# Kernel tuning notes

Hardware: AMD Instinct MI355X
Metric: run time of the kernel (lower is better)

The kernel has to match this reference:

```python
import jax, jax.numpy as jnp
import numpy as np

EMB_DIM = 768
N_WIRES = 10  # (768 - 1).bit_length()
DIM = 2 ** N_WIRES  # 1024
BATCH = 32
SENT_LEN = 128


def _cz_ring_sign(n):
    # Diagonal of (ring of adjacent CZ gates) @ CZ(0, n-1): -1 where an odd
    # number of the qubit pairs (k,k+1) for k<n-1 plus (0,n-1) are both |1>.
    idx = np.arange(2 ** n)
    bits = (idx[:, None] >> (n - 1 - np.arange(n))) & 1  # wire 0 = MSB (kron order)
    par = bits[:, 0] * bits[:, n - 1]
    for k in range(n - 1):
        par = par + bits[:, k] * bits[:, k + 1]
    return jnp.asarray(np.where(par % 2 == 1, -1.0, 1.0).astype(np.complex64))


_CZ_SIGN = _cz_ring_sign(N_WIRES)


def _apply_wire_gates(state, gates):
    # state: (batch, 2**n) complex64; gates: (n, 2, 2) complex64.
    # Contract each 2x2 gate onto its wire instead of building the 2^n x 2^n kron.
    n = gates.shape[0]
    b = state.shape[0]
    v = state.reshape((b,) + (2,) * n)
    for k in range(n):
        v = jnp.moveaxis(v, 1 + k, -1)
        v = v @ gates[k].T  # new_i = sum_j G[i, j] * old_j
        v = jnp.moveaxis(v, -1, 1 + k)
    return v.reshape(b, -1)


def _circuit(s, theta_x, theta_y):
    # [RXLayer, RYLayer, CZRing] repeated 3 times with SHARED parameters
    # (ModuleList([a,b,c]*3) reuses the same module instances).
    cx, sx = jnp.cos(theta_x), jnp.sin(theta_x)
    gx = jnp.stack([jnp.stack([cx, -1j * sx], -1),
                    jnp.stack([-1j * sx, cx], -1)], -2).astype(jnp.complex64)  # (n,2,2)
    cy, sy = jnp.cos(theta_y), jnp.sin(theta_y)
    gy = jnp.stack([jnp.stack([cy, -sy], -1),
                    jnp.stack([sy, cy], -1)], -2).astype(jnp.complex64)  # (n,2,2)
    for _ in range(3):
        s = _apply_wire_gates(s, gx)
        s = _apply_wire_gates(s, gy)
        s = s * _CZ_SIGN  # CZ ring + distant CZ(0, n-1) is diagonal
    return s


def setup_inputs() -> dict:
    key = jax.random.key(0)
    k1, k2, k3 = jax.random.split(key, 3)
    return {
        "x": jax.random.normal(k1, (BATCH, SENT_LEN, EMB_DIM), dtype=jnp.float32),
        "theta_x": jax.random.uniform(k2, (N_WIRES,), dtype=jnp.float32),
        "theta_y": jax.random.uniform(k3, (N_WIRES,), dtype=jnp.float32),
    }


def reference(x, theta_x, theta_y):
    xc = x.astype(jnp.complex64)
    pad = DIM - EMB_DIM
    s = jnp.pad(jnp.mean(xc, axis=1), ((0, 0), (0, pad)))  # (b, 2^n)
    ham = jnp.einsum('bsi,bsj->bij', xc, xc) / xc.shape[1]  # no conj, as in torch
    ham = jnp.pad(ham, ((0, 0), (0, pad), (0, pad)))  # (b, 2^n, 2^n)
    e = _circuit(s, theta_x, theta_y)  # (b, 2^n) complex
    scores = jnp.real(jnp.einsum('bi,bij,bj->b', e, ham, jnp.conj(e)))
    scores = jnp.clip(scores, 0.0, 1.0)
    return scores, e
```

## Files before the change

### kernel.cpp

```cpp
#include <hip/hip_runtime.h>

#define BATCH 32
#define SLEN  128
#define EMB   768
#define DIM   1024
#define NW    10

__global__ void __launch_bounds__(1024) fused_kernel(
        const float* __restrict__ x, const float* __restrict__ tx,
        const float* __restrict__ ty, float* __restrict__ out, int interleaved) {
    __shared__ float re[DIM], im[DIM];
    __shared__ float cx[NW], sx[NW], cy[NW], sy[NW];
    __shared__ float part[16];
    int b = blockIdx.x, t = threadIdx.x;

    if (t < NW) {
        float a = tx[t]; cx[t] = cosf(a); sx[t] = sinf(a);
        float c = ty[t]; cy[t] = cosf(c); sy[t] = sinf(c);
    }

    if (t < EMB) {
        const float* xp = x + (size_t)b * SLEN * EMB + t;
        float s0 = 0.f, s1 = 0.f, s2 = 0.f, s3 = 0.f;
        #pragma unroll 8
        for (int s = 0; s < SLEN; s += 4) {
            s0 += xp[(size_t)(s + 0) * EMB];
            s1 += xp[(size_t)(s + 1) * EMB];
            s2 += xp[(size_t)(s + 2) * EMB];
            s3 += xp[(size_t)(s + 3) * EMB];
        }
        re[t] = (s0 + s1 + s2 + s3) * (1.0f / SLEN);
    } else {
        re[t] = 0.f;
    }
    im[t] = 0.f;
    __syncthreads();

    for (int rep = 0; rep < 3; ++rep) {
        for (int k = 0; k < NW; ++k) {
            if (t < 512) {
                int p = 9 - k;
                int i0 = ((t >> p) << (p + 1)) | (t & ((1 << p) - 1));
                int i1 = i0 | (1 << p);
                float c = cx[k], s = sx[k];
                float r0 = re[i0], m0 = im[i0], r1 = re[i1], m1 = im[i1];
                re[i0] = c * r0 + s * m1;  im[i0] = c * m0 - s * r1;
                re[i1] = c * r1 + s * m0;  im[i1] = c * m1 - s * r0;
            }
            __syncthreads();
        }
        for (int k = 0; k < NW; ++k) {
            if (t < 512) {
                int p = 9 - k;
                int i0 = ((t >> p) << (p + 1)) | (t & ((1 << p) - 1));
                int i1 = i0 | (1 << p);
                float c = cy[k], s = sy[k];
                float r0 = re[i0], m0 = im[i0], r1 = re[i1], m1 = im[i1];
                re[i0] = c * r0 - s * r1;  im[i0] = c * m0 - s * m1;
                re[i1] = s * r0 + c * r1;  im[i1] = s * m0 + c * m1;
            }
            __syncthreads();
        }
        {
            int par = __popc((t & (t >> 1)) & 0x1FF) + ((t & (t >> 9)) & 1);
            if (par & 1) { re[t] = -re[t]; im[t] = -im[t]; }
        }
        __syncthreads();
    }

    float* e_out = out + BATCH;
    if (interleaved) {
        ((float2*)e_out)[b * DIM + t] = make_float2(re[t], im[t]);
    } else {
        e_out[b * DIM + t] = re[t];
    }

    int w = t >> 6, l = t & 63;
    float local = 0.f;
    for (int si = 0; si < 8; ++si) {
        int s = w * 8 + si;
        const float* xr = x + ((size_t)b * SLEN + s) * EMB;
        float du = 0.f, dv = 0.f;
        #pragma unroll
        for (int j = 0; j < 12; ++j) {
            float xv = xr[l + 64 * j];
            du += xv * re[l + 64 * j];
            dv += xv * im[l + 64 * j];
        }
        #pragma unroll
        for (int off = 32; off; off >>= 1) {
            du += __shfl_down(du, off, 64);
            dv += __shfl_down(dv, off, 64);
        }
        if (l == 0) local += du * du + dv * dv;
    }
    if (l == 0) part[w] = local;
    __syncthreads();
    if (t == 0) {
        float a = 0.f;
        #pragma unroll
        for (int i = 0; i < 16; ++i) a += part[i];
        out[b] = fminf(fmaxf(a * (1.0f / SLEN), 0.f), 1.f);
    }
}

extern "C" void kernel_launch(void* const* d_in, const int* in_sizes, int n_in,
                              void* d_out, int out_size, void* d_ws, size_t ws_size,
                              hipStream_t stream) {
    const float* x  = (const float*)d_in[0];
    const float* tx = (const float*)d_in[1];
    const float* ty = (const float*)d_in[2];
    float* out = (float*)d_out;

    int e_elems = out_size - BATCH;
    int interleaved = (e_elems >= BATCH * DIM * 2) ? 1 : 0;

    fused_kernel<<<BATCH, 1024, 0, stream>>>(x, tx, ty, out, interleaved);
}
```

Before: 87.14 us.

## Keep quantum state in registers and apply gates via wavefront shuffles with transposes

Each thread now holds one complex amplitude in registers. Gates on the five low-order qubits are applied with cross-lane shuffles, and the high-order qubits are handled by transposing the state through padded (skewed) shared memory. This replaces about 60 block-wide barriers per block with a few transpose barriers and halves idle threads. The final score loop also caches the state in registers instead of rereading shared memory. The cost is more complex index logic and relying on the wave64 shuffle width covering 32-lane groups.

Result: faster. 83.45 us (-4.2%).

```diff
diff --git a/kernel.cpp b/kernel.cpp
--- a/kernel.cpp
+++ b/kernel.cpp
@@ -6,19 +6,22 @@
 #define DIM   1024
 #define NW    10
 
+__device__ __forceinline__ int skew(int i) { return i + (i >> 5); }
+
 __global__ void __launch_bounds__(1024) fused_kernel(
         const float* __restrict__ x, const float* __restrict__ tx,
         const float* __restrict__ ty, float* __restrict__ out, int interleaved) {
-    __shared__ float re[DIM], im[DIM];
-    __shared__ float cx[NW], sx[NW], cy[NW], sy[NW];
+    __shared__ float2 st[DIM + DIM / 32];
+    __shared__ float cxs[NW], sxs[NW], cys[NW], sys[NW];
     __shared__ float part[16];
     int b = blockIdx.x, t = threadIdx.x;
 
     if (t < NW) {
-        float a = tx[t]; cx[t] = cosf(a); sx[t] = sinf(a);
-        float c = ty[t]; cy[t] = cosf(c); sy[t] = sinf(c);
+        float a = tx[t]; cxs[t] = cosf(a); sxs[t] = sinf(a);
+        float c = ty[t]; cys[t] = cosf(c); sys[t] = sinf(c);
     }
 
+    float r = 0.f, m = 0.f;
     if (t < EMB) {
         const float* xp = x + (size_t)b * SLEN * EMB + t;
         float s0 = 0.f, s1 = 0.f, s2 = 0.f, s3 = 0.f;
@@ -29,53 +32,77 @@
             s2 += xp[(size_t)(s + 2) * EMB];
             s3 += xp[(size_t)(s + 3) * EMB];
         }
-        re[t] = (s0 + s1 + s2 + s3) * (1.0f / SLEN);
-    } else {
-        re[t] = 0.f;
+        r = (s0 + s1 + s2 + s3) * (1.0f / SLEN);
     }
-    im[t] = 0.f;
     __syncthreads();
 
+    int tt = ((t & 31) << 5) | (t >> 5);
+
     for (int rep = 0; rep < 3; ++rep) {
-        for (int k = 0; k < NW; ++k) {
-            if (t < 512) {
-                int p = 9 - k;
-                int i0 = ((t >> p) << (p + 1)) | (t & ((1 << p) - 1));
-                int i1 = i0 | (1 << p);
-                float c = cx[k], s = sx[k];
-                float r0 = re[i0], m0 = im[i0], r1 = re[i1], m1 = im[i1];
-                re[i0] = c * r0 + s * m1;  im[i0] = c * m0 - s * r1;
-                re[i1] = c * r1 + s * m0;  im[i1] = c * m1 - s * r0;
-            }
-            __syncthreads();
+        #pragma unroll
+        for (int p = 0; p < 5; ++p) {
+            float c = cxs[9 - p], s = sxs[9 - p];
+            float pr = __shfl_xor(r, 1 << p, 64);
+            float pm = __shfl_xor(m, 1 << p, 64);
+            float nr = c * r + s * pm, nm = c * m - s * pr;
+            r = nr; m = nm;
         }
-        for (int k = 0; k < NW; ++k) {
-            if (t < 512) {
-                int p = 9 - k;
-                int i0 = ((t >> p) << (p + 1)) | (t & ((1 << p) - 1));
-                int i1 = i0 | (1 << p);
-                float c = cy[k], s = sy[k];
-                float r0 = re[i0], m0 = im[i0], r1 = re[i1], m1 = im[i1];
-                re[i0] = c * r0 - s * r1;  im[i0] = c * m0 - s * m1;
-                re[i1] = s * r0 + c * r1;  im[i1] = s * m0 + c * m1;
-            }
-            __syncthreads();
+        st[skew(t)] = make_float2(r, m);
+        __syncthreads();
+        { float2 v = st[skew(tt)]; r = v.x; m = v.y; }
+        #pragma unroll
+        for (int p = 5; p < 10; ++p) {
+            float c = cxs[9 - p], s = sxs[9 - p];
+            float pr = __shfl_xor(r, 1 << (p - 5), 64);
+            float pm = __shfl_xor(m, 1 << (p - 5), 64);
+            float nr = c * r + s * pm, nm = c * m - s * pr;
+            r = nr; m = nm;
         }
-        {
-            int par = __popc((t & (t >> 1)) & 0x1FF) + ((t & (t >> 9)) & 1);
-            if (par & 1) { re[t] = -re[t]; im[t] = -im[t]; }
+        #pragma unroll
+        for (int p = 5; p < 10; ++p) {
+            float c = cys[9 - p], s = sys[9 - p];
+            float pr = __shfl_xor(r, 1 << (p - 5), 64);
+            float pm = __shfl_xor(m, 1 << (p - 5), 64);
+            float sg = ((t >> (p - 5)) & 1) ? s : -s;
+            float nr = c * r + sg * pr, nm = c * m + sg * pm;
+            r = nr; m = nm;
         }
+        __syncthreads();
+        st[skew(tt)] = make_float2(r, m);
+        __syncthreads();
+        { float2 v = st[skew(t)]; r = v.x; m = v.y; }
+        #pragma unroll
+        for (int p = 0; p < 5; ++p) {
+            float c = cys[9 - p], s = sys[9 - p];
+            float pr = __shfl_xor(r, 1 << p, 64);
+            float pm = __shfl_xor(m, 1 << p, 64);
+            float sg = ((t >> p) & 1) ? s : -s;
+            float nr = c * r + sg * pr, nm = c * m + sg * pm;
+            r = nr; m = nm;
+        }
+        int par = __popc((t & (t >> 1)) & 0x1FF) + ((t >> 9) & t & 1);
+        if (par & 1) { r = -r; m = -m; }
         __syncthreads();
     }
 
     float* e_out = out + BATCH;
     if (interleaved) {
-        ((float2*)e_out)[b * DIM + t] = make_float2(re[t], im[t]);
+        ((float2*)e_out)[b * DIM + t] = make_float2(r, m);
     } else {
-        e_out[b * DIM + t] = re[t];
+        e_out[b * DIM + t] = r;
     }
 
+    st[skew(t)] = make_float2(r, m);
+    __syncthreads();
+
     int w = t >> 6, l = t & 63;
+    float ur[12], vr[12];
+    #pragma unroll
+    for (int j = 0; j < 12; ++j) {
+        float2 uv = st[skew(l + 64 * j)];
+        ur[j] = uv.x; vr[j] = uv.y;
+    }
+
     float local = 0.f;
     for (int si = 0; si < 8; ++si) {
         int s = w * 8 + si;
@@ -84,8 +111,8 @@
         #pragma unroll
         for (int j = 0; j < 12; ++j) {
             float xv = xr[l + 64 * j];
-            du += xv * re[l + 64 * j];
-            dv += xv * im[l + 64 * j];
+            du += xv * ur[j];
+            dv += xv * vr[j];
         }
         #pragma unroll
         for (int off = 32; off; off >>= 1) {
```
